# Optimization experiments

Measured on AMD Instinct MI355X. Metric: run time of the kernel, lower is better.

Reference implementation:

```python
import jax, jax.numpy as jnp
import numpy as np

N = 8192      # number of points
K = 64        # max_num_neighbors in radius()
C_IN = 64     # input feature channels
R = 0.125     # radius r


def setup_inputs() -> dict:
    key = jax.random.key(0)
    ks = jax.random.split(key, 8)
    s = 0.05
    return {
        "x": jax.random.normal(ks[0], (N, C_IN), jnp.float32),
        "pos": jax.random.uniform(ks[1], (N, 3), jnp.float32),
        "batch": jnp.zeros((N,), jnp.int32),
        "W1": jax.random.normal(ks[2], (C_IN + 3, 64), jnp.float32) * s,
        "b1": jnp.zeros((64,), jnp.float32),
        "W2": jax.random.normal(ks[3], (64, 128), jnp.float32) * s,
        "b2": jnp.zeros((128,), jnp.float32),
        "Wg": jax.random.normal(ks[4], (128, 256), jnp.float32) * s,
        "bg": jnp.zeros((256,), jnp.float32),
    }


def reference(x, pos, batch, W1, b1, W2, b2, Wg, bg):
    # --- radius neighbor search (K nearest within radius R, self included) ---
    sq = jnp.sum(pos * pos, axis=-1)                     # [N]
    d2 = sq[:, None] + sq[None, :] - 2.0 * (pos @ pos.T)  # [N, N] squared dists
    same = batch[:, None] == batch[None, :]
    d2 = jnp.where(same, d2, jnp.inf)
    neg_d2, idx = jax.lax.top_k(-d2, K)                  # [N, K] nearest K per target
    valid = (-neg_d2) <= R * R                           # within-radius mask; self always valid

    # --- PointConv message: feature_nn(concat(x_j, pos_j - pos_i)) ---
    rel = pos[idx] - pos[:, None, :]                     # [N, K, 3]
    feat = jnp.concatenate([x[idx], rel], axis=-1)       # [N, K, C_IN+3]
    h = jax.nn.relu(feat @ W1 + b1)                      # [N, K, 64]
    h = jax.nn.relu(h @ W2 + b2)                         # [N, K, 128]

    # --- max aggregation over neighbors ---
    h = jnp.where(valid[..., None], h, -jnp.inf)
    agg = jnp.max(h, axis=1)                             # [N, 128]

    # --- global_nn ---
    out = jax.nn.relu(agg @ Wg + bg)                     # [N, 256]
    return out
```

## Files before the change

### kernel.cpp

```cpp
#include <hip/hip_runtime.h>

#define N_PTS 8192
#define R2F 0.015625f

__global__ __launch_bounds__(256) void k_g(const float* __restrict__ x,
                                           const float* __restrict__ W1,
                                           float* __restrict__ g) {
    __shared__ float xs[32][68];
    __shared__ float ws_[64][64];
    const int t = threadIdx.x;
    const int r0 = blockIdx.x * 32;
    for (int v = t; v < 1024; v += 256)
        ((float4*)&ws_[0][0])[v] = ((const float4*)W1)[v];
    for (int v = t; v < 512; v += 256) {
        const int n = v >> 4, c4 = (v & 15) * 4;
        *(float4*)&xs[n][c4] = *(const float4*)&x[(r0 + n) * 64 + c4];
    }
    __syncthreads();
    const int c0 = (t & 15) * 4, n0 = (t >> 4) * 2;
    float acc[2][4];
    #pragma unroll
    for (int ni = 0; ni < 2; ++ni)
        #pragma unroll
        for (int ci = 0; ci < 4; ++ci) acc[ni][ci] = 0.0f;
    #pragma unroll
    for (int kb4 = 0; kb4 < 16; ++kb4) {
        float4 av[2], wv[4];
        #pragma unroll
        for (int ni = 0; ni < 2; ++ni)
            av[ni] = *(const float4*)&xs[n0 + ni][kb4 * 4];
        #pragma unroll
        for (int ki = 0; ki < 4; ++ki)
            wv[ki] = *(const float4*)&ws_[kb4 * 4 + ki][c0];
        #pragma unroll
        for (int ki = 0; ki < 4; ++ki) {
            #pragma unroll
            for (int ni = 0; ni < 2; ++ni) {
                const float a = (&av[ni].x)[ki];
                acc[ni][0] = __fmaf_rn(a, wv[ki].x, acc[ni][0]);
                acc[ni][1] = __fmaf_rn(a, wv[ki].y, acc[ni][1]);
                acc[ni][2] = __fmaf_rn(a, wv[ki].z, acc[ni][2]);
                acc[ni][3] = __fmaf_rn(a, wv[ki].w, acc[ni][3]);
            }
        }
    }
    #pragma unroll
    for (int ni = 0; ni < 2; ++ni)
        *(float4*)&g[(r0 + n0 + ni) * 64 + c0] =
            make_float4(acc[ni][0], acc[ni][1], acc[ni][2], acc[ni][3]);
}

__device__ __forceinline__ unsigned d2key(const float* __restrict__ pos, int j,
                                          float xi, float yi, float zi,
                                          float sqi) {
    const float xj = pos[j * 3 + 0], yj = pos[j * 3 + 1], zj = pos[j * 3 + 2];
    const float sqj = __fadd_rn(__fadd_rn(__fmul_rn(xj, xj), __fmul_rn(yj, yj)),
                                __fmul_rn(zj, zj));
    const float dot = __fmaf_rn(zi, zj, __fmaf_rn(yi, yj, __fmul_rn(xi, xj)));
    const float d2  = __fsub_rn(__fadd_rn(sqi, sqj), __fmul_rn(2.0f, dot));
    unsigned b = __float_as_uint(d2);
    return (b & 0x80000000u) ? ~b : (b | 0x80000000u);
}

union U0 {
    struct { unsigned mb[4][64]; unsigned mj[4][64]; } s;
    float gs[64][68];
};

__global__ __launch_bounds__(256, 5) void fused_all(const float* __restrict__ g,
                                                    const float* __restrict__ pos,
                                                    const float* __restrict__ W1,
                                                    const float* __restrict__ b1,
                                                    const float* __restrict__ W2,
                                                    const float* __restrict__ b2,
                                                    const float* __restrict__ Wg,
                                                    const float* __restrict__ bg,
                                                    float* __restrict__ out) {
    __shared__ U0    u0;
    __shared__ float pmw[4][128];
    __shared__ float aggS[128];
    __shared__ unsigned selb[64];
    __shared__ int   selj[64];
    __shared__ int   nvalidS;

    const int t    = threadIdx.x;
    const int lane = t & 63;
    const int w    = t >> 6;
    const int qb   = w << 11;
    const int i    = blockIdx.x;

    const float xi = pos[i * 3 + 0], yi = pos[i * 3 + 1], zi = pos[i * 3 + 2];
    const float sqi = __fadd_rn(__fadd_rn(__fmul_rn(xi, xi), __fmul_rn(yi, yi)),
                                __fmul_rn(zi, zi));

    unsigned m1b = 0xFFFFFFFFu, m2b = 0xFFFFFFFFu,
             m3b = 0xFFFFFFFFu, m4b = 0xFFFFFFFFu;
    int      m1j = 0x7FFFFFFF,  m2j = 0x7FFFFFFF,
             m3j = 0x7FFFFFFF,  m4j = 0x7FFFFFFF;
    #pragma unroll
    for (int k = 0; k < 32; ++k) {
        const int j = qb + lane + (k << 6);
        const unsigned b = d2key(pos, j, xi, yi, zi, sqi);
        if (b < m1b) {
            m4b = m3b; m4j = m3j; m3b = m2b; m3j = m2j;
            m2b = m1b; m2j = m1j; m1b = b;   m1j = j;
        } else if (b < m2b) {
            m4b = m3b; m4j = m3j; m3b = m2b; m3j = m2j;
            m2b = b;   m2j = j;
        } else if (b < m3b) {
            m4b = m3b; m4j = m3j; m3b = b;   m3j = j;
        } else if (b < m4b) {
            m4b = b;   m4j = j;
        }
    }

    u0.s.mb[w][lane] = 0xFFFFFFFFu;
    u0.s.mj[w][lane] = 0xFFFFFF00u | (unsigned)((w << 6) | lane);

    unsigned removed = 0u;
    int      level = 0;
    unsigned lb = m1b;
    int      lj = m1j;
    for (int s = 0; s < 64; ++s) {
        unsigned rb = lb;
        int      rj = lj;
        #pragma unroll
        for (int off = 32; off > 0; off >>= 1) {
            const unsigned ob = (unsigned)__shfl_down((int)rb, off);
            const int      oj = __shfl_down(rj, off);
            if (ob < rb || (ob == rb && oj < rj)) { rb = ob; rj = oj; }
        }
        const unsigned wb = (unsigned)__shfl((int)rb, 0);
        const int      wj = __shfl(rj, 0);
        const unsigned db = (wb & 0x80000000u) ? (wb ^ 0x80000000u) : ~wb;
        if (!(__uint_as_float(db) <= R2F)) break;
        if (lane == 0) { u0.s.mb[w][s] = wb; u0.s.mj[w][s] = (unsigned)wj; }
        if (lb == wb && lj == wj) {
            removed |= 1u << ((wj - qb - lane) >> 6);
            ++level;
            if      (level == 1) { lb = m2b; lj = m2j; }
            else if (level == 2) { lb = m3b; lj = m3j; }
            else if (level == 3) { lb = m4b; lj = m4j; }
            else {
                lb = 0xFFFFFFFFu; lj = 0x7FFFFFFF;
                #pragma unroll 4
                for (int k = 0; k < 32; ++k) {
                    if (!(removed & (1u << k))) {
                        const int jr = qb + lane + (k << 6);
                        const unsigned b = d2key(pos, jr, xi, yi, zi, sqi);
                        if (b < lb) { lb = b; lj = jr; }
                    }
                }
            }
        }
    }
    __syncthreads();

    {
        const int p = lane;
        const unsigned be = u0.s.mb[w][p];
        const unsigned je = u0.s.mj[w][p];
        int rank = p;
        #pragma unroll
        for (int d = 1; d < 4; ++d) {
            const int wp = (w + d) & 3;
            int lo = 0;
            #pragma unroll
            for (int st = 32; st > 0; st >>= 1) {
                const int idx = lo + st - 1;
                const unsigned ob = u0.s.mb[wp][idx];
                const unsigned oj = u0.s.mj[wp][idx];
                if (ob < be || (ob == be && oj < je)) lo += st;
            }
            {
                const unsigned ob = u0.s.mb[wp][lo];
                const unsigned oj = u0.s.mj[wp][lo];
                if (ob < be || (ob == be && oj < je)) lo += 1;
            }
            rank += lo;
        }
        if (rank < 64) { selb[rank] = be; selj[rank] = (int)(je & 8191u); }
    }
    __syncthreads();

    for (int v = t; v < 1024; v += 256) {
        const int n = v >> 4, c4 = (v & 15) * 4;
        *(float4*)&u0.gs[n][c4] = *(const float4*)&g[selj[n] * 64 + c4];
    }
    {
        bool ok = false;
        if (t < 64) {
            const unsigned b = selb[t];
            const unsigned db = (b & 0x80000000u) ? (b ^ 0x80000000u) : ~b;
            ok = (__uint_as_float(db) <= R2F);
        }
        const unsigned long long vm = __ballot(ok);
        if (t == 0) nvalidS = __popcll(vm);
    }
    __syncthreads();
    const int nvalid = nvalidS;

    {
        const int c0 = (t & 15) * 4, n0 = (t >> 4) * 4;
        float rr[4][3];
        #pragma unroll
        for (int ni = 0; ni < 4; ++ni) {
            const int j = selj[n0 + ni];
            rr[ni][0] = pos[j * 3 + 0] - xi;
            rr[ni][1] = pos[j * 3 + 1] - yi;
            rr[ni][2] = pos[j * 3 + 2] - zi;
        }
        float w1b[3][4], bb[4];
        #pragma unroll
        for (int ci = 0; ci < 4; ++ci) {
            w1b[0][ci] = W1[4096 + c0 + ci];
            w1b[1][ci] = W1[4160 + c0 + ci];
            w1b[2][ci] = W1[4224 + c0 + ci];
            bb[ci]     = b1[c0 + ci];
        }
        #pragma unroll
        for (int ni = 0; ni < 4; ++ni) {
            const int n = n0 + ni;
            const float4 gv = *(const float4*)&u0.gs[n][c0];
            float4 hv;
            #pragma unroll
            for (int ci = 0; ci < 4; ++ci) {
                float a = (&gv.x)[ci];
                a = __fmaf_rn(rr[ni][0], w1b[0][ci], a);
                a = __fmaf_rn(rr[ni][1], w1b[1][ci], a);
                a = __fmaf_rn(rr[ni][2], w1b[2][ci], a);
                a = fmaxf(a + bb[ci], 0.0f);
                (&hv.x)[ci] = (n < nvalid) ? a : 0.0f;
            }
            *(float4*)&u0.gs[n][c0] = hv;
        }
    }
    __syncthreads();

    {
        const float (*h1)[68] = u0.gs;
        const int c4 = (t & 15) * 4;
        const int nb = (t >> 4) * 4;
        #pragma unroll
        for (int half = 0; half < 2; ++half) {
            const int ch0 = half * 64 + c4;
            float acc[4][4];
            #pragma unroll
            for (int ni = 0; ni < 4; ++ni)
                #pragma unroll
                for (int k = 0; k < 4; ++k) acc[ni][k] = 0.0f;

            #pragma unroll 2
            for (int ccb = 0; ccb < 16; ++ccb) {
                #pragma unroll
                for (int pr = 0; pr < 2; ++pr) {
                    const int cc0 = ccb * 4 + pr * 2;
                    const float4 wt0 = *(const float4*)&W2[(cc0 + 0) * 128 + ch0];
                    const float4 wt1 = *(const float4*)&W2[(cc0 + 1) * 128 + ch0];
                    #pragma unroll
                    for (int ni = 0; ni < 4; ++ni) {
                        const float2 av = *(const float2*)&h1[nb + ni][cc0];
                        acc[ni][0] = __fmaf_rn(av.x, wt0.x, acc[ni][0]);
                        acc[ni][1] = __fmaf_rn(av.x, wt0.y, acc[ni][1]);
                        acc[ni][2] = __fmaf_rn(av.x, wt0.z, acc[ni][2]);
                        acc[ni][3] = __fmaf_rn(av.x, wt0.w, acc[ni][3]);
                        acc[ni][0] = __fmaf_rn(av.y, wt1.x, acc[ni][0]);
                        acc[ni][1] = __fmaf_rn(av.y, wt1.y, acc[ni][1]);
                        acc[ni][2] = __fmaf_rn(av.y, wt1.z, acc[ni][2]);
                        acc[ni][3] = __fmaf_rn(av.y, wt1.w, acc[ni][3]);
                    }
                }
            }
            float m4v[4];
            #pragma unroll
            for (int k = 0; k < 4; ++k) {
                const float bb = b2[ch0 + k];
                float mm = 0.0f;
                #pragma unroll
                for (int ni = 0; ni < 4; ++ni)
                    if (nb + ni < nvalid) mm = fmaxf(mm, acc[ni][k] + bb);
                m4v[k] = mm;
            }
            #pragma unroll
            for (int k = 0; k < 4; ++k) {
                float v = m4v[k];
                v = fmaxf(v, __shfl_down(v, 32));
                v = fmaxf(v, __shfl_down(v, 16));
                m4v[k] = v;
            }
            if ((t & 63) < 16) {
                #pragma unroll
                for (int k = 0; k < 4; ++k) pmw[w][ch0 + k] = m4v[k];
            }
        }
    }
    __syncthreads();

    if (t < 128)
        aggS[t] = fmaxf(fmaxf(pmw[0][t], pmw[1][t]),
                        fmaxf(pmw[2][t], pmw[3][t]));
    __syncthreads();

    {
        float acc = 0.0f;
        #pragma unroll 8
        for (int k = 0; k < 128; ++k)
            acc = __fmaf_rn(aggS[k], Wg[k * 256 + t], acc);
        out[i * 256 + t] = fmaxf(acc + bg[t], 0.0f);
    }
}

extern "C" void kernel_launch(void* const* d_in, const int* in_sizes, int n_in,
                              void* d_out, int out_size, void* d_ws, size_t ws_size,
                              hipStream_t stream) {
    const float* x   = (const float*)d_in[0];
    const float* pos = (const float*)d_in[1];
    const float* W1 = (const float*)d_in[3];
    const float* b1 = (const float*)d_in[4];
    const float* W2 = (const float*)d_in[5];
    const float* b2 = (const float*)d_in[6];
    const float* Wg = (const float*)d_in[7];
    const float* bg = (const float*)d_in[8];
    float* out = (float*)d_out;

    float* g = (float*)d_ws;

    k_g<<<N_PTS / 32, 256, 0, stream>>>(x, W1, g);
    fused_all<<<N_PTS, 256, 0, stream>>>(g, pos, W1, b1, W2, b2, Wg, bg, out);
}
```

Measured before the change: 388.3 us.

## Split fused kernel into neighbor-select and MLP kernels via output scratch

Result: faster. 380.5 us (-2.0%).

```diff
diff --git a/kernel.cpp b/kernel.cpp
--- a/kernel.cpp
+++ b/kernel.cpp
@@ -62,26 +62,10 @@
     return (b & 0x80000000u) ? ~b : (b | 0x80000000u);
 }
 
-union U0 {
-    struct { unsigned mb[4][64]; unsigned mj[4][64]; } s;
-    float gs[64][68];
-};
-
-__global__ __launch_bounds__(256, 5) void fused_all(const float* __restrict__ g,
-                                                    const float* __restrict__ pos,
-                                                    const float* __restrict__ W1,
-                                                    const float* __restrict__ b1,
-                                                    const float* __restrict__ W2,
-                                                    const float* __restrict__ b2,
-                                                    const float* __restrict__ Wg,
-                                                    const float* __restrict__ bg,
-                                                    float* __restrict__ out) {
-    __shared__ U0    u0;
-    __shared__ float pmw[4][128];
-    __shared__ float aggS[128];
-    __shared__ unsigned selb[64];
-    __shared__ int   selj[64];
-    __shared__ int   nvalidS;
+__global__ __launch_bounds__(256, 8) void k_sel(const float* __restrict__ pos,
+                                                float* __restrict__ out) {
+    __shared__ unsigned mb[4][64];
+    __shared__ unsigned mj[4][64];
 
     const int t    = threadIdx.x;
     const int lane = t & 63;
@@ -114,8 +98,8 @@
         }
     }
 
-    u0.s.mb[w][lane] = 0xFFFFFFFFu;
-    u0.s.mj[w][lane] = 0xFFFFFF00u | (unsigned)((w << 6) | lane);
+    mb[w][lane] = 0xFFFFFFFFu;
+    mj[w][lane] = 0xFFFFFF00u | (unsigned)((w << 6) | lane);
 
     unsigned removed = 0u;
     int      level = 0;
@@ -134,7 +118,7 @@
         const int      wj = __shfl(rj, 0);
         const unsigned db = (wb & 0x80000000u) ? (wb ^ 0x80000000u) : ~wb;
         if (!(__uint_as_float(db) <= R2F)) break;
-        if (lane == 0) { u0.s.mb[w][s] = wb; u0.s.mj[w][s] = (unsigned)wj; }
+        if (lane == 0) { mb[w][s] = wb; mj[w][s] = (unsigned)wj; }
         if (lb == wb && lj == wj) {
             removed |= 1u << ((wj - qb - lane) >> 6);
             ++level;
@@ -158,8 +142,8 @@
 
     {
         const int p = lane;
-        const unsigned be = u0.s.mb[w][p];
-        const unsigned je = u0.s.mj[w][p];
+        const unsigned be = mb[w][p];
+        const unsigned je = mj[w][p];
         int rank = p;
         #pragma unroll
         for (int d = 1; d < 4; ++d) {
@@ -168,32 +152,60 @@
             #pragma unroll
             for (int st = 32; st > 0; st >>= 1) {
                 const int idx = lo + st - 1;
-                const unsigned ob = u0.s.mb[wp][idx];
-                const unsigned oj = u0.s.mj[wp][idx];
+                const unsigned ob = mb[wp][idx];
+                const unsigned oj = mj[wp][idx];
                 if (ob < be || (ob == be && oj < je)) lo += st;
             }
             {
-                const unsigned ob = u0.s.mb[wp][lo];
-                const unsigned oj = u0.s.mj[wp][lo];
+                const unsigned ob = mb[wp][lo];
+                const unsigned oj = mj[wp][lo];
                 if (ob < be || (ob == be && oj < je)) lo += 1;
             }
             rank += lo;
         }
-        if (rank < 64) { selb[rank] = be; selj[rank] = (int)(je & 8191u); }
+        if (rank < 64) {
+            const unsigned db = (be & 0x80000000u) ? (be ^ 0x80000000u) : ~be;
+            const bool ok = (__uint_as_float(db) <= R2F);
+            ((ushort*)(out + (size_t)i * 256))[rank] =
+                (ushort)((je & 8191u) | (ok ? 0x8000u : 0u));
+        }
+    }
+}
+
+__global__ __launch_bounds__(256, 5) void k_mlp(const float* __restrict__ g,
+                                                const float* __restrict__ pos,
+                                                const float* __restrict__ W1,
+                                                const float* __restrict__ b1,
+                                                const float* __restrict__ W2,
+                                                const float* __restrict__ b2,
+                                                const float* __restrict__ Wg,
+                                                const float* __restrict__ bg,
+                                                float* __restrict__ out) {
+    __shared__ float gs[64][68];
+    __shared__ float pmw[4][128];
+    __shared__ float aggS[128];
+    __shared__ int   selj[64];
+    __shared__ int   nvalidS;
+
+    const int t = threadIdx.x;
+    const int w = t >> 6;
+    const int i = blockIdx.x;
+
+    const float xi = pos[i * 3 + 0], yi = pos[i * 3 + 1], zi = pos[i * 3 + 2];
+
+    bool ok = false;
+    if (t < 64) {
+        const unsigned sv = ((const ushort*)(out + (size_t)i * 256))[t];
+        selj[t] = (int)(sv & 8191u);
+        ok = (sv & 0x8000u) != 0u;
     }
     __syncthreads();
 
     for (int v = t; v < 1024; v += 256) {
         const int n = v >> 4, c4 = (v & 15) * 4;
-        *(float4*)&u0.gs[n][c4] = *(const float4*)&g[selj[n] * 64 + c4];
-    }
-    {
-        bool ok = false;
-        if (t < 64) {
-            const unsigned b = selb[t];
-            const unsigned db = (b & 0x80000000u) ? (b ^ 0x80000000u) : ~b;
-            ok = (__uint_as_float(db) <= R2F);
-        }
+        *(float4*)&gs[n][c4] = *(const float4*)&g[selj[n] * 64 + c4];
+    }
+    {
         const unsigned long long vm = __ballot(ok);
         if (t == 0) nvalidS = __popcll(vm);
     }
@@ -221,7 +233,7 @@
         #pragma unroll
         for (int ni = 0; ni < 4; ++ni) {
             const int n = n0 + ni;
-            const float4 gv = *(const float4*)&u0.gs[n][c0];
+            const float4 gv = *(const float4*)&gs[n][c0];
             float4 hv;
             #pragma unroll
             for (int ci = 0; ci < 4; ++ci) {
@@ -232,13 +244,13 @@
                 a = fmaxf(a + bb[ci], 0.0f);
                 (&hv.x)[ci] = (n < nvalid) ? a : 0.0f;
             }
-            *(float4*)&u0.gs[n][c0] = hv;
-        }
-    }
-    __syncthreads();
-
-    {
-        const float (*h1)[68] = u0.gs;
+            *(float4*)&gs[n][c0] = hv;
+        }
+    }
+    __syncthreads();
+
+    {
+        const float (*h1)[68] = gs;
         const int c4 = (t & 15) * 4;
         const int nb = (t >> 4) * 4;
         #pragma unroll
@@ -326,5 +338,6 @@
     float* g = (float*)d_ws;
 
     k_g<<<N_PTS / 32, 256, 0, stream>>>(x, W1, g);
-    fused_all<<<N_PTS, 256, 0, stream>>>(g, pos, W1, b1, W2, b2, Wg, bg, out);
-}
+    k_sel<<<N_PTS, 256, 0, stream>>>(pos, out);
+    k_mlp<<<N_PTS, 256, 0, stream>>>(g, pos, W1, b1, W2, b2, Wg, bg, out);
+}
```
